# Kernel tuning notes

Hardware: AMD Instinct MI355X
Metric: run time of the kernel (lower is better)

The kernel has to match this reference:

```python
import jax, jax.numpy as jnp
import numpy as np

N_NODES, N_EDGES, N_REL, F_DIM, N_HEAD, N_LAYERS = 20000, 100000, 1000, 128, 4, 4
NEG_SLOPE = 0.2  # PyG GATv2Conv default negative_slope


def _gatv2_layer(x, ea_full, src, dst, Wl, bl, Wr, br, We, att, bias):
    # x: [N, F]; ea_full: [Etot, F] edge attrs (incl. self-loop rows)
    N = x.shape[0]
    H, C = att.shape  # heads, out-dim per head
    xl = (x @ Wl + bl).reshape(N, H, C)          # source-side projection
    xr = (x @ Wr + br).reshape(N, H, C)          # target-side projection
    ee = (ea_full @ We).reshape(-1, H, C)        # [Etot, H, C] edge embedding
    # GATv2 scoring: leaky_relu(x_i + x_j + e) . att
    e = jax.nn.leaky_relu(xl[src] + xr[dst] + ee, NEG_SLOPE)
    logits = jnp.einsum('ehc,hc->eh', e, att)    # [Etot, H]
    # segment softmax over edges grouped by destination node
    m = jax.ops.segment_max(logits, dst, num_segments=N)
    p = jnp.exp(logits - m[dst])
    denom = jax.ops.segment_sum(p, dst, num_segments=N)
    alpha = p / denom[dst]                       # [Etot, H]
    out = jax.ops.segment_sum(alpha[:, :, None] * xl[src], dst, num_segments=N)
    return out.mean(axis=1) + bias               # concat=False -> head mean


def setup_inputs() -> dict:
    key = jax.random.key(0)
    ks = jax.random.split(key, 12)
    N, E, R, F, H, L = N_NODES, N_EDGES, N_REL, F_DIM, N_HEAD, N_LAYERS
    HC = H * F
    s = 1.0 / np.sqrt(F)
    return {
        'x': jax.random.normal(ks[0], (N, F), jnp.float32),
        'edge_index': jax.random.randint(ks[1], (2, E), 0, N, dtype=jnp.int32),
        'relations': jax.random.normal(ks[2], (R, F), jnp.float32),
        'relation_index': jax.random.randint(ks[3], (E,), 0, R, dtype=jnp.int32),
        'Wl': jax.random.normal(ks[4], (L, F, HC), jnp.float32) * s,
        'bl': jnp.zeros((L, HC), jnp.float32),
        'Wr': jax.random.normal(ks[5], (L, F, HC), jnp.float32) * s,
        'br': jnp.zeros((L, HC), jnp.float32),
        'We': jax.random.normal(ks[6], (L, F, HC), jnp.float32) * s,
        'att': jax.random.normal(ks[7], (L, H, F), jnp.float32) * s,
        'bias': jnp.zeros((L, F), jnp.float32),
    }


def reference(x, edge_index, relations, relation_index, Wl, bl, Wr, br, We, att, bias):
    N = x.shape[0]
    sl = jnp.arange(N, dtype=edge_index.dtype)
    src = jnp.concatenate([edge_index[0], sl])   # add_self_loops=True
    dst = jnp.concatenate([edge_index[1], sl])
    ea = relations[relation_index]               # [E, F]
    # self-loop edge_attr uses fill_value='mean' (PyG default)
    ea_mean = ea.mean(axis=0)
    ea_full = jnp.concatenate([ea, jnp.broadcast_to(ea_mean, (N, ea.shape[1]))])
    h = x
    for l in range(N_LAYERS):
        h = _gatv2_layer(h, ea_full, src, dst, Wl[l], bl[l], Wr[l], br[l], We[l], att[l], bias[l])
    return (h, relations)
```

## Files before the change

### kernel.cpp

```cpp
#include <hip/hip_runtime.h>
#include <hip/hip_bf16.h>

#define N_NODES   20000
#define N_EDGES   100000
#define N_REL     1000
#define F_DIM     128
#define N_HEAD    4
#define HC        512
#define HC2       256
#define N_LAYERS  4
#define REL_EXT_ROWS 1008
#define NEG_SLOPE 0.2f
#define NODE_MB   ((N_NODES + 63) / 64)
#define REL_MB    ((REL_EXT_ROWS + 63) / 64)

typedef __attribute__((ext_vector_type(8))) short short8;
typedef __attribute__((ext_vector_type(4))) float floatx4;

__device__ __forceinline__ float loadIn(const void* p, size_t i, int f32) {
    if (f32) return ((const float*)p)[i];
    union { unsigned int u; float f; } c;
    c.u = ((unsigned int)((const unsigned short*)p)[i]) << 16;
    return c.f;
}

__device__ __forceinline__ unsigned short f2bf(float v) {
    __hip_bfloat16 b = __float2bfloat16(v);
    return *(unsigned short*)&b;
}

__device__ __forceinline__ void unpack2(unsigned int u, float& lo, float& hi) {
    union { unsigned int u; float f; } a, b;
    a.u = u << 16;
    b.u = u & 0xFFFF0000u;
    lo = a.f; hi = b.f;
}

__device__ __forceinline__ void unpack8(uint4 v, float* f) {
    unpack2(v.x, f[0], f[1]);
    unpack2(v.y, f[2], f[3]);
    unpack2(v.z, f[4], f[5]);
    unpack2(v.w, f[6], f[7]);
}

__global__ void detect_kernel(const unsigned short* __restrict__ x, int* __restrict__ flag) {
    int t = threadIdx.x;
    int cnt = 0;
    for (int j = t; j < 256; j += 64) {
        int e = (x[j] >> 7) & 0xFF;
        if (e >= 143) cnt++;
    }
    for (int off = 32; off; off >>= 1) cnt += __shfl_xor(cnt, off);
    if (t == 0) flag[0] = (cnt >= 8) ? 1 : 0;
}


__global__ void hist_kernel(const int* __restrict__ dst, const int* __restrict__ rel,
                            int* __restrict__ deg, int* __restrict__ rcount) {
    int e = blockIdx.x * 256 + threadIdx.x;
    if (e < N_EDGES) {
        atomicAdd(&deg[dst[e]], 1);
        atomicAdd(&rcount[rel[e]], 1);
    }
}

__global__ void ea_mean_kernel(const int* __restrict__ rcount,
                               const void* __restrict__ relations,
                               float* __restrict__ ea_mean, const int* __restrict__ flag) {
    int f32 = flag[0];
    int b = blockIdx.x;
    int t = threadIdx.x;
    int col = t & 127;
    int rhalf = t >> 7;
    float acc = 0.f;
    for (int j = 0; j < 4; ++j) {
        int r = b * 8 + j * 2 + rhalf;
        acc += (float)rcount[r] * loadIn(relations, (size_t)r * F_DIM + col, f32);
    }
    __shared__ float part[256];
    part[t] = acc;
    __syncthreads();
    if (t < 128)
        atomicAdd(&ea_mean[col], (part[t] + part[t + 128]) * (1.f / (float)N_EDGES));
}

__global__ void relext_kernel(const void* __restrict__ relations,
                              const float* __restrict__ ea_mean,
                              unsigned short* __restrict__ rel_ext, const int* __restrict__ flag) {
    int idx = blockIdx.x * 256 + threadIdx.x;
    if (idx >= REL_EXT_ROWS * F_DIM) return;
    int f32 = flag[0];
    int r = idx >> 7;
    int c = idx & 127;
    float v;
    if (r < N_REL)       v = loadIn(relations, idx, f32);
    else if (r == N_REL) v = ea_mean[c];
    else                 v = 0.f;
    rel_ext[idx] = f2bf(v);
}

__global__ void scan_kernel(const int* __restrict__ deg,
                            int* __restrict__ row_start, int* __restrict__ cursor) {
    __shared__ int part[1024];
    int t = threadIdx.x;
    const int CH = (N_NODES + 1023) / 1024;
    int base = t * CH;
    int sum = 0;
    for (int j = 0; j < CH; ++j) {
        int idx = base + j;
        if (idx < N_NODES) sum += deg[idx];
    }
    part[t] = sum;
    __syncthreads();
    for (int off = 1; off < 1024; off <<= 1) {
        int u = (t >= off) ? part[t - off] : 0;
        __syncthreads();
        part[t] += u;
        __syncthreads();
    }
    int run = part[t] - sum;
    for (int j = 0; j < CH; ++j) {
        int idx = base + j;
        if (idx < N_NODES) {
            row_start[idx] = run;
            cursor[idx] = run;
            run += deg[idx];
        }
    }
    if (t == 1023) row_start[N_NODES] = part[1023];
}

__global__ void scatter_kernel(const int* __restrict__ src, const int* __restrict__ dst,
                               const int* __restrict__ rel, int* __restrict__ cursor,
                               int* __restrict__ csr_pack) {
    int e = blockIdx.x * 256 + threadIdx.x;
    if (e < N_EDGES) {
        int d = dst[e];
        int p = atomicAdd(&cursor[d], 1);
        csr_pack[p] = src[e] | (rel[e] << 16);
    }
}

__global__ void build8_kernel(const int* __restrict__ row_start,
                              const int* __restrict__ csr_pack,
                              int* __restrict__ csr8) {
    int i = blockIdx.x * 256 + threadIdx.x;
    if (i >= N_NODES) return;
    int rs = row_start[i];
    int deg = row_start[i + 1] - rs;
    if (deg < 0) deg = 0;
    int dcap = deg > 4095 ? 4095 : deg;
    csr8[i * 8] = rs | (dcap << 17);
    #pragma unroll
    for (int k = 0; k < 7; ++k)
        csr8[i * 8 + 1 + k] = (k < deg) ? csr_pack[rs + k] : 0;
}

__global__ void tail_kernel(const void* __restrict__ relations, void* __restrict__ out,
                            const int* __restrict__ flag) {
    int i = blockIdx.x * 256 + threadIdx.x;
    if (i >= N_REL * F_DIM) return;
    int f32 = flag[0];
    float v = loadIn(relations, i, f32);
    size_t o = (size_t)N_NODES * F_DIM + i;
    if (f32) ((float*)out)[o] = v;
    else     ((unsigned short*)out)[o] = f2bf(v);
}

__global__ void w_transpose_kernel(const void* __restrict__ Wl, const void* __restrict__ Wr,
                                   const void* __restrict__ We,
                                   unsigned short* __restrict__ Wt, const int* __restrict__ flag) {
    int f32 = flag[0];
    int k0 = blockIdx.x * 64;
    int n0 = blockIdx.y * 64;
    int mat = blockIdx.z;
    const void* src = (mat < 4) ? Wl : (mat < 8 ? Wr : We);
    size_t base = (size_t)(mat & 3) * F_DIM * HC;
    unsigned short* dst = Wt + (size_t)mat * HC * F_DIM;
    __shared__ float T[64][65];
    int t = threadIdx.x;
    int r = t >> 2, cq = t & 3;
    for (int j = 0; j < 16; ++j) {
        int n = cq * 16 + j;
        T[n][r] = loadIn(src, base + (size_t)(k0 + r) * HC + n0 + n, f32);
    }
    __syncthreads();
    for (int j = 0; j < 16; ++j) {
        int k = cq * 16 + j;
        dst[(size_t)(n0 + r) * F_DIM + k0 + k] = f2bf(T[r][k]);
    }
}

__launch_bounds__(256, 4)
__global__ void proj_kernel(const void* __restrict__ A_node, int a_input,
                            const unsigned short* __restrict__ rel_ext,
                            const unsigned short* __restrict__ Wlt,
                            const unsigned short* __restrict__ Wrt,
                            const unsigned short* __restrict__ Wet,
                            const void* __restrict__ bl, const void* __restrict__ br,
                            size_t boff,
                            unsigned short* __restrict__ xl,
                            unsigned short* __restrict__ xr,
                            unsigned short* __restrict__ re,
                            const int* __restrict__ flag) {
    __shared__ __align__(16) short As[64][136];
    __shared__ __align__(16) short BtRaw[128 * 72];
    int f32 = flag[0];
    int isNode = (blockIdx.x < NODE_MB);
    int m0 = (isNode ? blockIdx.x : (blockIdx.x - NODE_MB)) * 64;
    int M = isNode ? N_NODES : REL_EXT_ROWS;
    int tpb = isNode ? 2 : 1;
    int a_f32 = (isNode && a_input) ? f32 : 0;
    const void* A = isNode ? A_node : (const void*)rel_ext;
    int t = threadIdx.x;

    for (int j = 0; j < 4; ++j) {
        int c = t + j * 256;
        int row = c >> 4;
        int colc = (c & 15) * 8;
        int gm = m0 + row;
        short8 v = (short8){0, 0, 0, 0, 0, 0, 0, 0};
        if (gm < M) {
            size_t idx = (size_t)gm * F_DIM + colc;
            if (a_f32) {
                const float* Af = (const float*)A;
                for (int q = 0; q < 8; ++q) v[q] = (short)f2bf(Af[idx + q]);
            } else {
                v = *(const short8*)((const unsigned short*)A + idx);
            }
        }
        *(short8*)&As[row][colc] = v;
    }

    int wave = t >> 6, lane = t & 63;
    int wm = (wave >> 1) * 32, wn = (wave & 1) * 64;
    int r16 = lane & 15, quad = lane >> 4;

    for (int it = 0; it < tpb; ++it) {
        int nt = isNode ? (blockIdx.y * 2 + it) : blockIdx.y;
        const unsigned short* Wt = isNode ? ((nt < 4) ? Wlt : Wrt) : Wet;
        int n0 = (nt & 3) * 128;

        floatx4 acc[2][4];
        for (int mi = 0; mi < 2; ++mi)
            for (int ni = 0; ni < 4; ++ni)
                acc[mi][ni] = (floatx4){0.f, 0.f, 0.f, 0.f};

        for (int half = 0; half < 2; ++half) {
            __syncthreads();
            for (int j = 0; j < 4; ++j) {
                int c = t + j * 256;
                int nl = c >> 3;
                int kc = (c & 7) * 8;
                *(short8*)&BtRaw[nl * 72 + kc] =
                    *(const short8*)(Wt + (size_t)(n0 + nl) * F_DIM + half * 64 + kc);
            }
            __syncthreads();

            for (int kk = 0; kk < 2; ++kk) {
                short8 a[2], b[4];
                for (int mi = 0; mi < 2; ++mi)
                    a[mi] = *(const short8*)&As[wm + mi * 16 + r16][half * 64 + kk * 32 + quad * 8];
                for (int ni = 0; ni < 4; ++ni)
                    b[ni] = *(const short8*)&BtRaw[(wn + ni * 16 + r16) * 72 + kk * 32 + quad * 8];
                for (int mi = 0; mi < 2; ++mi)
                    for (int ni = 0; ni < 4; ++ni)
                        acc[mi][ni] = __builtin_amdgcn_mfma_f32_16x16x32_bf16(a[mi], b[ni], acc[mi][ni], 0, 0, 0);
            }
        }

        const void* bias = isNode ? ((nt < 4) ? bl : br) : nullptr;
        unsigned short* out = isNode ? ((nt < 4) ? xl : xr) : re;
        __syncthreads();
        for (int mi = 0; mi < 2; ++mi) {
            for (int ni = 0; ni < 4; ++ni) {
                int col = wn + ni * 16 + r16;
                float bv = bias ? loadIn(bias, boff + n0 + col, f32) : 0.f;
                for (int r = 0; r < 4; ++r) {
                    int rowl = wm + mi * 16 + quad * 4 + r;
                    BtRaw[rowl * 136 + col] = (short)f2bf(acc[mi][ni][r] + bv);
                }
            }
        }
        __syncthreads();
        for (int j = 0; j < 4; ++j) {
            int c = t + j * 256;
            int rowl = c >> 4;
            int colc = (c & 15) * 8;
            int gm = m0 + rowl;
            if (gm < M)
                *(short8*)(out + (size_t)gm * HC + n0 + colc) =
                    *(const short8*)&BtRaw[rowl * 136 + colc];
        }
    }
}

__launch_bounds__(128)
__global__ void edge_kernel(const unsigned int* __restrict__ xl2,
                            const unsigned int* __restrict__ xr2,
                            const unsigned int* __restrict__ re2,
                            const int* __restrict__ csr8,
                            const int* __restrict__ csr_pack,
                            const void* __restrict__ att, size_t att_off,
                            const void* __restrict__ bias, size_t bias_off,
                            void* __restrict__ hout, int final_layer,
                            const int* __restrict__ flag) {
    int f32 = flag[0];
    int wid = threadIdx.x >> 6;
    int lane = threadIdx.x & 63;
    int i = blockIdx.x * 2 + wid;
    if (i >= N_NODES) return;
    int h = lane >> 4;
    int q = lane & 15;
    int loff = h * 64 + q * 4;

    uint4 h0 = *(const uint4*)(csr8 + (size_t)i * 8);
    uint4 h1 = *(const uint4*)(csr8 + (size_t)i * 8 + 4);
    int rs  = (int)(h0.x & 0x1FFFF);
    int deg = (int)(h0.x >> 17) & 0xFFF;
    int ew[7] = { (int)h0.y, (int)h0.z, (int)h0.w, (int)h1.x, (int)h1.y, (int)h1.z, (int)h1.w };

    float xr[8];
    { uint4 v = *(const uint4*)(xr2 + (size_t)i * HC2 + loff); unpack8(v, xr); }
    float er[8];
    { uint4 v = *(const uint4*)(re2 + (size_t)N_REL * HC2 + loff); unpack8(v, er); }
    float av[8];
    #pragma unroll
    for (int j = 0; j < 8; ++j)
        av[j] = loadIn(att, att_off + (size_t)h * F_DIM + q * 8 + j, f32);

    int nIn = deg > 7 ? 7 : deg;
    uint4 xv[7], rv[7];
    #pragma unroll
    for (int k = 0; k < 7; ++k) {
        if (k < nIn) {
            int pk = ew[k];
            int sn = pk & 0xFFFF;        if (sn >= N_NODES) sn = 0;
            int rn = (pk >> 16) & 0x3FF; if (rn > N_REL) rn = N_REL;
            xv[k] = *(const uint4*)(xl2 + (size_t)sn * HC2 + loff);
            rv[k] = *(const uint4*)(re2 + (size_t)rn * HC2 + loff);
        }
    }

    float acc[8];
    float s;
    {
        float xs[8];
        uint4 v = *(const uint4*)(xl2 + (size_t)i * HC2 + loff);
        unpack8(v, xs);
        float part = 0.f;
        #pragma unroll
        for (int j = 0; j < 8; ++j) {
            float u = xs[j] + xr[j] + er[j];
            u = fmaxf(u, NEG_SLOPE * u);
            part = fmaf(u, av[j], part);
        }
        #pragma unroll
        for (int off = 8; off; off >>= 1) part += __shfl_xor(part, off);
        part = fminf(fmaxf(part, -60.f), 60.f);
        float p = __expf(part);
        s = p;
        #pragma unroll
        for (int j = 0; j < 8; ++j) acc[j] = p * xs[j];
    }

    #pragma unroll
    for (int k = 0; k < 7; ++k) {
        if (k < nIn) {
            float xlv[8], ee[8];
            unpack8(xv[k], xlv);
            unpack8(rv[k], ee);
            float part = 0.f;
            #pragma unroll
            for (int j = 0; j < 8; ++j) {
                float u = xlv[j] + xr[j] + ee[j];
                u = fmaxf(u, NEG_SLOPE * u);
                part = fmaf(u, av[j], part);
            }
            #pragma unroll
            for (int off = 8; off; off >>= 1) part += __shfl_xor(part, off);
            part = fminf(fmaxf(part, -60.f), 60.f);
            float pp = __expf(part);
            s += pp;
            #pragma unroll
            for (int j = 0; j < 8; ++j) acc[j] = fmaf(pp, xlv[j], acc[j]);
        }
    }

    if (deg > 7) {
        int e1 = rs + deg;
        if (e1 > N_EDGES) e1 = N_EDGES;
        for (int b = rs + 7; b < e1; b += 4) {
            int nb = e1 - b; if (nb > 4) nb = 4;
            uint4 xo[4], ro[4];
            #pragma unroll
            for (int k = 0; k < 4; ++k) {
                if (k < nb) {
                    int pk = csr_pack[b + k];
                    int sn = pk & 0xFFFF;        if (sn >= N_NODES) sn = 0;
                    int rn = (pk >> 16) & 0x3FF; if (rn > N_REL) rn = N_REL;
                    xo[k] = *(const uint4*)(xl2 + (size_t)sn * HC2 + loff);
                    ro[k] = *(const uint4*)(re2 + (size_t)rn * HC2 + loff);
                }
            }
            #pragma unroll
            for (int k = 0; k < 4; ++k) {
                if (k < nb) {
                    float xlv[8], ee[8];
                    unpack8(xo[k], xlv);
                    unpack8(ro[k], ee);
                    float part = 0.f;
                    #pragma unroll
                    for (int j = 0; j < 8; ++j) {
                        float u = xlv[j] + xr[j] + ee[j];
                        u = fmaxf(u, NEG_SLOPE * u);
                        part = fmaf(u, av[j], part);
                    }
                    #pragma unroll
                    for (int off = 8; off; off >>= 1) part += __shfl_xor(part, off);
                    part = fminf(fmaxf(part, -60.f), 60.f);
                    float pp = __expf(part);
                    s += pp;
                    #pragma unroll
                    for (int j = 0; j < 8; ++j) acc[j] = fmaf(pp, xlv[j], acc[j]);
                }
            }
        }
    }

    float inv = 1.f / s;
    float outv[8];
    #pragma unroll
    for (int j = 0; j < 8; ++j) outv[j] = acc[j] * inv;
    #pragma unroll
    for (int j = 0; j < 8; ++j) {
        outv[j] += __shfl_xor(outv[j], 16);
        outv[j] += __shfl_xor(outv[j], 32);
    }

    if (h == 0) {
        float bv[8];
        #pragma unroll
        for (int j = 0; j < 8; ++j)
            bv[j] = loadIn(bias, bias_off + q * 8 + j, f32);
        size_t o = (size_t)i * F_DIM + q * 8;
        if (final_layer && f32) {
            float* op = (float*)hout + o;
            float4 lo, hi;
            lo.x = outv[0] * 0.25f + bv[0];
            lo.y = outv[1] * 0.25f + bv[1];
            lo.z = outv[2] * 0.25f + bv[2];
            lo.w = outv[3] * 0.25f + bv[3];
            hi.x = outv[4] * 0.25f + bv[4];
            hi.y = outv[5] * 0.25f + bv[5];
            hi.z = outv[6] * 0.25f + bv[6];
            hi.w = outv[7] * 0.25f + bv[7];
            *(float4*)op = lo;
            *(float4*)(op + 4) = hi;
        } else {
            unsigned int w[4];
            #pragma unroll
            for (int p = 0; p < 4; ++p) {
                float v0 = outv[2 * p] * 0.25f + bv[2 * p];
                float v1 = outv[2 * p + 1] * 0.25f + bv[2 * p + 1];
                w[p] = (unsigned int)f2bf(v0) | ((unsigned int)f2bf(v1) << 16);
            }
            *(uint4*)((unsigned short*)hout + o) = *(uint4*)w;
        }
    }
}


extern "C" void kernel_launch(void* const* d_in, const int* in_sizes, int n_in,
                              void* d_out, int out_size, void* d_ws, size_t ws_size,
                              hipStream_t stream) {
    const void* x          = d_in[0];
    const int*  edge_index = (const int*)d_in[1];
    const void* relations  = d_in[2];
    const int*  rel_index  = (const int*)d_in[3];
    const void* Wl         = d_in[4];
    const void* bl         = d_in[5];
    const void* Wr         = d_in[6];
    const void* br         = d_in[7];
    const void* We         = d_in[8];
    const void* att        = d_in[9];
    const void* bias       = d_in[10];

    char* ws = (char*)d_ws;
    size_t off = 0;
    auto alloc = [&](size_t bytes) -> void* {
        void* p = ws + off;
        off = (off + bytes + 255) & ~(size_t)255;
        return p;
    };
    int*            flag     = (int*)alloc(4);
    char*           zero0    = ws + off;
    int*            deg      = (int*)alloc(N_NODES * 4);
    int*            rcount   = (int*)alloc(N_REL * 4);
    float*          ea_mean  = (float*)alloc(F_DIM * 4);
    size_t          zlen     = (size_t)((ws + off) - zero0);
    int*            row_start= (int*)alloc((N_NODES + 1) * 4);
    int*            cursor   = (int*)alloc(N_NODES * 4);
    int*            csr_pack = (int*)alloc(N_EDGES * 4);
    int*            csr8     = (int*)alloc((size_t)N_NODES * 8 * 4);
    unsigned short* rel_ext  = (unsigned short*)alloc((size_t)REL_EXT_ROWS * F_DIM * 2);
    unsigned short* Wt       = (unsigned short*)alloc((size_t)12 * HC * F_DIM * 2);
    unsigned short* re       = (unsigned short*)alloc((size_t)REL_EXT_ROWS * HC * 2);
    unsigned short* hbuf     = (unsigned short*)alloc((size_t)N_NODES * F_DIM * 2);
    unsigned short* xl       = (unsigned short*)alloc((size_t)N_NODES * HC * 2);
    unsigned short* xr       = (unsigned short*)alloc((size_t)N_NODES * HC * 2);

    const int* esrc = edge_index;
    const int* edst = edge_index + N_EDGES;

    detect_kernel<<<1, 64, 0, stream>>>((const unsigned short*)x, flag);
    hipMemsetAsync(zero0, 0, zlen, stream);
    hist_kernel<<<(N_EDGES + 255) / 256, 256, 0, stream>>>(edst, rel_index, deg, rcount);
    ea_mean_kernel<<<N_REL / 8, 256, 0, stream>>>(rcount, relations, ea_mean, flag);
    relext_kernel<<<(REL_EXT_ROWS * F_DIM + 255) / 256, 256, 0, stream>>>(relations, ea_mean, rel_ext, flag);
    scan_kernel<<<1, 1024, 0, stream>>>(deg, row_start, cursor);
    scatter_kernel<<<(N_EDGES + 255) / 256, 256, 0, stream>>>(esrc, edst, rel_index, cursor, csr_pack);
    build8_kernel<<<(N_NODES + 255) / 256, 256, 0, stream>>>(row_start, csr_pack, csr8);
    w_transpose_kernel<<<dim3(2, 8, 12), 256, 0, stream>>>(Wl, Wr, We, Wt, flag);
    tail_kernel<<<(N_REL * F_DIM + 255) / 256, 256, 0, stream>>>(relations, d_out, flag);

    const void* hin = x;
    int a_input = 1;
    for (int l = 0; l < N_LAYERS; ++l) {
        const unsigned short* Wlt = Wt + (size_t)l * HC * F_DIM;
        const unsigned short* Wrt = Wt + (size_t)(4 + l) * HC * F_DIM;
        const unsigned short* Wet = Wt + (size_t)(8 + l) * HC * F_DIM;
        proj_kernel<<<dim3(NODE_MB + REL_MB, 4), 256, 0, stream>>>(
            hin, a_input, rel_ext, Wlt, Wrt, Wet,
            bl, br, (size_t)l * HC,
            xl, xr, re, flag);
        int final_layer = (l == N_LAYERS - 1);
        void* hout = final_layer ? d_out : (void*)hbuf;
        edge_kernel<<<(N_NODES + 1) / 2, 128, 0, stream>>>(
            (const unsigned int*)xl, (const unsigned int*)xr, (const unsigned int*)re,
            csr8, csr_pack,
            att, (size_t)l * N_HEAD * F_DIM,
            bias, (size_t)l * F_DIM,
            hout, final_layer, flag);
        hin = hbuf;
        a_input = 0;
    }
}
```

Measured before the change: 416.8 us.

## Keep weight tile in registers and loop over row tiles in projection GEMM

Restructures the projection kernel so each block owns one 128-column weight slice, held in registers for the whole block, and iterates over several 64-row A tiles, prefetching the next A tile into registers while the current one computes. The per-half weight staging through shared memory and its barriers go away, and the grid is remapped to 159x8 blocks with relation rows handled in 256-row chunks. The cost is higher register pressure (launch bounds lowered to 3 blocks per SM) and fewer blocks per output column.

New measurement: 423.7 us. About the same (+1.7%).

```diff
diff --git a/kernel.cpp b/kernel.cpp
--- a/kernel.cpp
+++ b/kernel.cpp
@@ -11,8 +11,7 @@
 #define N_LAYERS  4
 #define REL_EXT_ROWS 1008
 #define NEG_SLOPE 0.2f
-#define NODE_MB   ((N_NODES + 63) / 64)
-#define REL_MB    ((REL_EXT_ROWS + 63) / 64)
+#define PROJ_NODE_X 157
 
 typedef __attribute__((ext_vector_type(8))) short short8;
 typedef __attribute__((ext_vector_type(4))) float floatx4;
@@ -191,7 +190,7 @@
     }
 }
 
-__launch_bounds__(256, 4)
+__launch_bounds__(256, 3)
 __global__ void proj_kernel(const void* __restrict__ A_node, int a_input,
                             const unsigned short* __restrict__ rel_ext,
                             const unsigned short* __restrict__ Wlt,
@@ -204,21 +203,60 @@
                             unsigned short* __restrict__ re,
                             const int* __restrict__ flag) {
     __shared__ __align__(16) short As[64][136];
-    __shared__ __align__(16) short BtRaw[128 * 72];
+    __shared__ __align__(16) short Cs[64 * 136];
     int f32 = flag[0];
-    int isNode = (blockIdx.x < NODE_MB);
-    int m0 = (isNode ? blockIdx.x : (blockIdx.x - NODE_MB)) * 64;
-    int M = isNode ? N_NODES : REL_EXT_ROWS;
-    int tpb = isNode ? 2 : 1;
-    int a_f32 = (isNode && a_input) ? f32 : 0;
-    const void* A = isNode ? A_node : (const void*)rel_ext;
     int t = threadIdx.x;
-
+    int y = blockIdx.y;
+    int isNode = (blockIdx.x < PROJ_NODE_X);
+
+    const void* A;
+    const unsigned short* Wt;
+    const void* bias;
+    unsigned short* out;
+    int M, mbase, nT, a_f32;
+    int n0 = (y & 3) * 128;
+    if (isNode) {
+        A = A_node; M = N_NODES; nT = 2;
+        mbase = blockIdx.x * 128;
+        a_f32 = a_input ? f32 : 0;
+        if (y < 4) { Wt = Wlt; bias = bl; out = xl; }
+        else       { Wt = Wrt; bias = br; out = xr; }
+    } else {
+        A = (const void*)rel_ext; M = REL_EXT_ROWS; nT = 4;
+        int rowchunk = (blockIdx.x - PROJ_NODE_X) * 2 + (y >> 2);
+        mbase = rowchunk * 256;
+        a_f32 = 0;
+        Wt = Wet; bias = nullptr; out = re;
+    }
+
+    int wave = t >> 6, lane = t & 63;
+    int wm = (wave >> 1) * 32, wn = (wave & 1) * 64;
+    int r16 = lane & 15, quad = lane >> 4;
+
+    short8 breg[2][2][4];
+    #pragma unroll
+    for (int half = 0; half < 2; ++half)
+        #pragma unroll
+        for (int kk = 0; kk < 2; ++kk)
+            #pragma unroll
+            for (int ni = 0; ni < 4; ++ni)
+                breg[half][kk][ni] = *(const short8*)(
+                    Wt + (size_t)(n0 + wn + ni * 16 + r16) * F_DIM + half * 64 + kk * 32 + quad * 8);
+
+    float bv[4];
+    #pragma unroll
+    for (int ni = 0; ni < 4; ++ni)
+        bv[ni] = bias ? loadIn(bias, boff + n0 + wn + ni * 16 + r16, f32) : 0.f;
+
+    int sRow = 0, sCol = 0;
+
+    short8 aS[4];
+    #pragma unroll
     for (int j = 0; j < 4; ++j) {
         int c = t + j * 256;
         int row = c >> 4;
         int colc = (c & 15) * 8;
-        int gm = m0 + row;
+        int gm = mbase + row;
         short8 v = (short8){0, 0, 0, 0, 0, 0, 0, 0};
         if (gm < M) {
             size_t idx = (size_t)gm * F_DIM + colc;
@@ -229,60 +267,82 @@
                 v = *(const short8*)((const unsigned short*)A + idx);
             }
         }
-        *(short8*)&As[row][colc] = v;
-    }
-
-    int wave = t >> 6, lane = t & 63;
-    int wm = (wave >> 1) * 32, wn = (wave & 1) * 64;
-    int r16 = lane & 15, quad = lane >> 4;
-
-    for (int it = 0; it < tpb; ++it) {
-        int nt = isNode ? (blockIdx.y * 2 + it) : blockIdx.y;
-        const unsigned short* Wt = isNode ? ((nt < 4) ? Wlt : Wrt) : Wet;
-        int n0 = (nt & 3) * 128;
+        aS[j] = v;
+    }
+    (void)sRow; (void)sCol;
+
+    for (int ct = 0; ct < nT; ++ct) {
+        int m0 = mbase + ct * 64;
+        __syncthreads();
+        #pragma unroll
+        for (int j = 0; j < 4; ++j) {
+            int c = t + j * 256;
+            *(short8*)&As[c >> 4][(c & 15) * 8] = aS[j];
+        }
+        short8 aN[4];
+        if (ct + 1 < nT) {
+            int mb = mbase + (ct + 1) * 64;
+            #pragma unroll
+            for (int j = 0; j < 4; ++j) {
+                int c = t + j * 256;
+                int row = c >> 4;
+                int colc = (c & 15) * 8;
+                int gm = mb + row;
+                short8 v = (short8){0, 0, 0, 0, 0, 0, 0, 0};
+                if (gm < M) {
+                    size_t idx = (size_t)gm * F_DIM + colc;
+                    if (a_f32) {
+                        const float* Af = (const float*)A;
+                        for (int q = 0; q < 8; ++q) v[q] = (short)f2bf(Af[idx + q]);
+                    } else {
+                        v = *(const short8*)((const unsigned short*)A + idx);
+                    }
+                }
+                aN[j] = v;
+            }
+            #pragma unroll
+            for (int j = 0; j < 4; ++j) aS[j] = aN[j];
+        }
+        __syncthreads();
 
         floatx4 acc[2][4];
+        #pragma unroll
         for (int mi = 0; mi < 2; ++mi)
+            #pragma unroll
             for (int ni = 0; ni < 4; ++ni)
                 acc[mi][ni] = (floatx4){0.f, 0.f, 0.f, 0.f};
 
+        #pragma unroll
         for (int half = 0; half < 2; ++half) {
-            __syncthreads();
-            for (int j = 0; j < 4; ++j) {
-                int c = t + j * 256;
-                int nl = c >> 3;
-                int kc = (c & 7) * 8;
-                *(short8*)&BtRaw[nl * 72 + kc] =
-                    *(const short8*)(Wt + (size_t)(n0 + nl) * F_DIM + half * 64 + kc);
-            }
-            __syncthreads();
-
+            #pragma unroll
             for (int kk = 0; kk < 2; ++kk) {
-                short8 a[2], b[4];
+                short8 a[2];
+                #pragma unroll
                 for (int mi = 0; mi < 2; ++mi)
                     a[mi] = *(const short8*)&As[wm + mi * 16 + r16][half * 64 + kk * 32 + quad * 8];
-                for (int ni = 0; ni < 4; ++ni)
-                    b[ni] = *(const short8*)&BtRaw[(wn + ni * 16 + r16) * 72 + kk * 32 + quad * 8];
+                #pragma unroll
                 for (int mi = 0; mi < 2; ++mi)
+                    #pragma unroll
                     for (int ni = 0; ni < 4; ++ni)
-                        acc[mi][ni] = __builtin_amdgcn_mfma_f32_16x16x32_bf16(a[mi], b[ni], acc[mi][ni], 0, 0, 0);
-            }
-        }
-
-        const void* bias = isNode ? ((nt < 4) ? bl : br) : nullptr;
-        unsigned short* out = isNode ? ((nt < 4) ? xl : xr) : re;
-        __syncthreads();
+                        acc[mi][ni] = __builtin_amdgcn_mfma_f32_16x16x32_bf16(
+                            a[mi], breg[half][kk][ni], acc[mi][ni], 0, 0, 0);
+            }
+        }
+
+        #pragma unroll
         for (int mi = 0; mi < 2; ++mi) {
+            #pragma unroll
             for (int ni = 0; ni < 4; ++ni) {
                 int col = wn + ni * 16 + r16;
-                float bv = bias ? loadIn(bias, boff + n0 + col, f32) : 0.f;
+                #pragma unroll
                 for (int r = 0; r < 4; ++r) {
                     int rowl = wm + mi * 16 + quad * 4 + r;
-                    BtRaw[rowl * 136 + col] = (short)f2bf(acc[mi][ni][r] + bv);
+                    Cs[rowl * 136 + col] = (short)f2bf(acc[mi][ni][r] + bv[ni]);
                 }
             }
         }
         __syncthreads();
+        #pragma unroll
         for (int j = 0; j < 4; ++j) {
             int c = t + j * 256;
             int rowl = c >> 4;
@@ -290,7 +350,7 @@
             int gm = m0 + rowl;
             if (gm < M)
                 *(short8*)(out + (size_t)gm * HC + n0 + colc) =
-                    *(const short8*)&BtRaw[rowl * 136 + colc];
+                    *(const short8*)&Cs[rowl * 136 + colc];
         }
     }
 }
@@ -530,7 +590,7 @@
         const unsigned short* Wlt = Wt + (size_t)l * HC * F_DIM;
         const unsigned short* Wrt = Wt + (size_t)(4 + l) * HC * F_DIM;
         const unsigned short* Wet = Wt + (size_t)(8 + l) * HC * F_DIM;
-        proj_kernel<<<dim3(NODE_MB + REL_MB, 4), 256, 0, stream>>>(
+        proj_kernel<<<dim3(PROJ_NODE_X + 2, 8), 256, 0, stream>>>(
             hin, a_input, rel_ext, Wlt, Wrt, Wet,
             bl, br, (size_t)l * HC,
             xl, xr, re, flag);
```
